# Kernel optimization log

Hardware: AMD Instinct MI355X
Metric: run time of the kernel (lower is better)

The kernel has to match this reference:

```python
import jax, jax.numpy as jnp
import numpy as np

B, N, D, HEAD = 16, 1024, 512, 256  # hidden_size=512, gcn_layer=2 -> head_dim=256


def _xavier(key, shape):
    lim = (6.0 / (shape[0] + shape[-1])) ** 0.5
    return jax.random.uniform(key, shape, jnp.float32, -lim, lim)


def setup_inputs() -> dict:
    key = jax.random.key(0)
    ks = jax.random.split(key, 10)
    fi_lim = (6.0 / (D + 1)) ** 0.5
    return {
        "x": jax.random.normal(ks[0], (B, N, D), jnp.float32),
        "tp_w": _xavier(ks[1], (D, D)), "tp_b": jnp.zeros((D,), jnp.float32),
        "tc_w": _xavier(ks[2], (D, D)), "tc_b": jnp.zeros((D,), jnp.float32),
        "fi_w": jax.random.uniform(ks[3], (D,), jnp.float32, -fi_lim, fi_lim),
        "bil_w": _xavier(ks[4], (D, D)),
        "gcn_w0": _xavier(ks[5], (D, HEAD)), "gcn_b0": jnp.zeros((HEAD,), jnp.float32),
        "gcn_w1": _xavier(ks[6], (D + HEAD, HEAD)), "gcn_b1": jnp.zeros((HEAD,), jnp.float32),
        "out_w": _xavier(ks[7], (D, D)), "out_b": jnp.zeros((D,), jnp.float32),
    }


def reference(x, tp_w, tp_b, tc_w, tc_b, fi_w, bil_w,
              gcn_w0, gcn_b0, gcn_w1, gcn_b1, out_w, out_b):
    Bb, Nn, Dd = x.shape
    # ---- StructInduction: matrix-tree latent structure ----
    tp = jnp.tanh(x @ tp_w + tp_b)                      # [B,N,D]
    tc = jnp.tanh(x @ tc_w + tc_b)                      # [B,N,D]
    # original expands BOTH tp and tc along dim 2 -> f_ij[b,i,j] = s[b,i]
    s = jnp.einsum('bnd,de,bne->bn', tp, bil_w, tc)     # [B,N]
    f_i = jnp.exp(x @ fi_w)                             # [B,N] root scores
    eye = jnp.eye(Nn, dtype=x.dtype)
    A = jnp.exp(s)[:, :, None] * (1.0 - eye)            # [B,N,N], zero diagonal
    col_sum = A.sum(axis=1)                             # [B,N] sum over dim 1
    L = -A + col_sum[:, None, :] * eye                  # Laplacian
    L = L.at[:, 0, :].set(f_i)                          # replace row 0 with root scores
    Linv = jnp.linalg.inv(L)                            # [B,N,N]
    d0 = f_i * Linv[:, :, 0]                            # [B,N]
    diag = jnp.diagonal(Linv, axis1=-2, axis2=-1)       # [B,N]
    tmp1 = A * diag[:, None, :]                         # A[b,i,j]*Linv_diag[b,j]
    tmp2 = A * jnp.swapaxes(Linv, 1, 2)                 # A[b,i,j]*Linv[b,j,i]
    mask1 = jnp.concatenate([jnp.zeros((Nn, 1), x.dtype),
                             jnp.ones((Nn, Nn - 1), x.dtype)], axis=1)  # zero col 0
    mask2 = mask1.T                                     # zero row 0
    dx = mask1 * tmp1 - mask2 * tmp2                    # [B,N,N]
    d = jnp.concatenate([d0[:, None, :], dx], axis=1)   # [B,N+1,N]
    df = jnp.swapaxes(d, 1, 2)                          # [B,N,N+1]
    adj = df[:, :, 1:]                                  # [B,N,N] latent adjacency
    # ---- GraphConvLayer (self_loop=True, dropout = identity / eval) ----
    denom = adj.sum(axis=2, keepdims=True) + 1.0        # [B,N,1]
    outputs = x
    cache = [x]
    outs = []
    for (W, b) in ((gcn_w0, gcn_b0), (gcn_w1, gcn_b1)):
        Ax = adj @ outputs                              # [B,N,in_dim]
        AxW = (Ax @ W + b) + (outputs @ W + b)          # neighbor + self loop
        g = jax.nn.relu(AxW / denom)                    # [B,N,HEAD]
        cache.append(g)
        outputs = jnp.concatenate(cache, axis=2)        # densely connected
        outs.append(g)
    gcn_out = jnp.concatenate(outs, axis=2) + x         # [B,N,D] residual
    return gcn_out @ out_w + out_b
```

## Files before the change

kernel.cpp:

```cpp
#include <hip/hip_runtime.h>
#include <cmath>

#define BN   16384
#define DD   512
#define HEADN 256

typedef unsigned short ushort;
typedef short short8 __attribute__((ext_vector_type(8)));
typedef float floatx4 __attribute__((ext_vector_type(4)));
typedef unsigned short ushort4v __attribute__((ext_vector_type(4)));
typedef unsigned short ushort8v __attribute__((ext_vector_type(8)));

__device__ __forceinline__ ushort f2bf(float v) {
    unsigned int u = __float_as_uint(v);
    unsigned int r = u + 0x7FFFu + ((u >> 16) & 1u);
    return (ushort)(r >> 16);
}
__device__ __forceinline__ float bf2f(ushort u) {
    return __uint_as_float(((unsigned int)u) << 16);
}
__device__ __forceinline__ float tanh_fast(float x) {
    float xc = fminf(fmaxf(x, -15.0f), 15.0f);
    float e = __expf(2.0f * xc);
    return (e - 1.0f) * __builtin_amdgcn_rcpf(e + 1.0f);
}

template <int TM, int TN, int BK, int KK, int EPI>
__global__ __launch_bounds__(256) void gemm_lds(
    const ushort* __restrict__ A, int lda,
    const ushort* __restrict__ Bt, int N,
    const float* __restrict__ bias,
    const float* __restrict__ denom,
    const ushort* __restrict__ tcb, int tcld,
    float* __restrict__ s_arr,
    void* __restrict__ Cout, int ldc,
    const ushort* __restrict__ xgb, int xoff, ushort* __restrict__ gout)
{
    constexpr int WGM = (TN == 64 && TM == 128) ? 4 : 2;
    constexpr int WGN = 4 / WGM;
    constexpr int MI = TM / (WGM * 16);
    constexpr int NI = TN / (WGN * 16);
    constexpr int KSTEPS = BK / 32;
    constexpr int ROWS = TM + TN;
    constexpr int CPR = BK / 8;
    constexpr int CPT = (ROWS * CPR) / 256;
    constexpr int MT = 16384 / TM;
    constexpr int MT_PER_BAND = MT / 8;
    constexpr int NK = KK / BK;
    __shared__ ushort S[2 * ROWS * BK];

    const int g = blockIdx.x;
    const int band = g & 7, within = g >> 3;
    const int nt = within / MT_PER_BAND;
    const int mt = band * MT_PER_BAND + (within - nt * MT_PER_BAND);
    const int m0 = mt * TM, n0 = nt * TN;
    const int w = threadIdx.x >> 6, L = threadIdx.x & 63;
    const int wr0 = ((WGN == 2) ? (w >> 1) : w) * (MI * 16);
    const int wc0 = ((WGN == 2) ? (w & 1) : 0) * (NI * 16);
    const int lrow = L & 15, quad = L >> 4;

    const ushort* gbase[CPT];
#pragma unroll
    for (int rr = 0; rr < CPT; ++rr) {
        const int chunk = rr * 256 + (w << 6) + L;
        const int row = chunk / CPR, slot = chunk % CPR;
        const int ca = slot ^ ((row >> 1) & (CPR - 1));
        gbase[rr] = (row < TM)
            ? A  + (size_t)(m0 + row) * lda    + (ca << 3)
            : Bt + (size_t)(n0 + row - TM) * KK + (ca << 3);
    }

    floatx4 zero4 = {0.0f, 0.0f, 0.0f, 0.0f};
    floatx4 acc[MI][NI];
#pragma unroll
    for (int i = 0; i < MI; ++i)
#pragma unroll
        for (int j = 0; j < NI; ++j) acc[i][j] = zero4;

    auto stage = [&](int buf, int k0) {
        ushort* Sd = S + buf * (ROWS * BK);
#pragma unroll
        for (int rr = 0; rr < CPT; ++rr) {
            __builtin_amdgcn_global_load_lds(
                (const __attribute__((address_space(1))) unsigned int*)(gbase[rr] + k0),
                (__attribute__((address_space(3))) unsigned int*)(Sd + (rr * 256 + (w << 6)) * 8),
                16, 0, 0);
        }
    };

    stage(0, 0);
#pragma unroll
    for (int kk = 0; kk < NK; ++kk) {
        __syncthreads();
        if (kk + 1 < NK) stage((kk + 1) & 1, (kk + 1) * BK);

        const ushort* Sc = S + (kk & 1) * (ROWS * BK);
        short8 af[KSTEPS][MI], bfr[KSTEPS][NI];
#pragma unroll
        for (int ks = 0; ks < KSTEPS; ++ks) {
#pragma unroll
            for (int mi = 0; mi < MI; ++mi) {
                const int row = wr0 + (mi << 4) + lrow;
                const int slot = ((ks << 2) + quad) ^ ((row >> 1) & (CPR - 1));
                af[ks][mi] = *(const short8*)(Sc + row * BK + (slot << 3));
            }
#pragma unroll
            for (int ni = 0; ni < NI; ++ni) {
                const int row = TM + wc0 + (ni << 4) + lrow;
                const int slot = ((ks << 2) + quad) ^ ((row >> 1) & (CPR - 1));
                bfr[ks][ni] = *(const short8*)(Sc + row * BK + (slot << 3));
            }
        }
#pragma unroll
        for (int ks = 0; ks < KSTEPS; ++ks)
#pragma unroll
            for (int mi = 0; mi < MI; ++mi)
#pragma unroll
                for (int ni = 0; ni < NI; ++ni)
                    acc[mi][ni] = __builtin_amdgcn_mfma_f32_16x16x32_bf16(
                        af[ks][mi], bfr[ks][ni], acc[mi][ni], 0, 0, 0);
    }

    if constexpr (EPI == 3) {
#pragma unroll
        for (int mi = 0; mi < MI; ++mi) {
            float rs[4] = {0.f, 0.f, 0.f, 0.f};
#pragma unroll
            for (int ni = 0; ni < NI; ++ni) {
                const int gc = n0 + wc0 + (ni << 4) + lrow;
#pragma unroll
                for (int p = 0; p < 4; ++p) {
                    const int gr = m0 + wr0 + (mi << 4) + (quad << 2) + p;
                    rs[p] += acc[mi][ni][p] * bf2f(tcb[(size_t)gr * tcld + gc]);
                }
            }
#pragma unroll
            for (int p = 0; p < 4; ++p)
#pragma unroll
                for (int o = 1; o < 16; o <<= 1) rs[p] += __shfl_xor(rs[p], o);
            if (lrow == 0) {
#pragma unroll
                for (int p = 0; p < 4; ++p)
                    atomicAdd(s_arr + m0 + wr0 + (mi << 4) + (quad << 2) + p, rs[p]);
            }
        }
    } else {
#pragma unroll
        for (int mi = 0; mi < MI; ++mi) {
#pragma unroll
            for (int p = 0; p < 4; ++p) {
                const int gr = m0 + wr0 + (mi << 4) + (quad << 2) + p;
                const float rdv = (EPI == 2) ? __builtin_amdgcn_rcpf(denom[gr]) : 1.0f;
#pragma unroll
                for (int ni = 0; ni < NI; ++ni) {
                    const int gc = n0 + wc0 + (ni << 4) + lrow;
                    const float v = acc[mi][ni][p];
                    if constexpr (EPI == 0) {
                        ((float*)Cout)[(size_t)gr * ldc + gc] = v + bias[gc];
                    } else if constexpr (EPI == 1) {
                        ((ushort*)Cout)[(size_t)gr * ldc + gc] = f2bf(tanh_fast(v + bias[gc]));
                    } else {
                        float u = (v + 2.0f * bias[gc]) * rdv;
                        u = u > 0.0f ? u : 0.0f;
                        if (Cout)
                            ((ushort*)Cout)[(size_t)gr * ldc + gc] = f2bf(u);
                        if (gout)
                            gout[(size_t)gr * 512 + xoff + gc] =
                                f2bf(u + bf2f(xgb[(size_t)gr * 512 + xoff + gc]));
                    }
                }
            }
        }
    }
}

__global__ __launch_bounds__(256) void prep_k(
    const float* __restrict__ x, const float* __restrict__ fiw,
    ushort* __restrict__ xb, float* __restrict__ fdot,
    const float* __restrict__ tp_w, const float* __restrict__ tc_w,
    const float* __restrict__ bilw, const float* __restrict__ ow,
    const float* __restrict__ w0, const float* __restrict__ w1,
    const float* __restrict__ tp_b, const float* __restrict__ tc_b,
    ushort* __restrict__ tptcwT, ushort* __restrict__ bilwT,
    ushort* __restrict__ owT, ushort* __restrict__ w0T,
    ushort* __restrict__ w1T, float* __restrict__ bias2)
{
    const int blk0 = blockIdx.x;
    if (blk0 < 4096) {
        const int wv = threadIdx.x >> 6, L = threadIdx.x & 63;
        const int r = (blk0 << 2) + wv;
        const float* xr = x + (size_t)r * DD;
        const int c0 = L << 3;
        float4 v0 = *(const float4*)(xr + c0);
        float4 v1 = *(const float4*)(xr + c0 + 4);
        float4 f0 = *(const float4*)(fiw + c0);
        float4 f1 = *(const float4*)(fiw + c0 + 4);
        float d = v0.x * f0.x + v0.y * f0.y + v0.z * f0.z + v0.w * f0.w
                + v1.x * f1.x + v1.y * f1.y + v1.z * f1.z + v1.w * f1.w;
        ushort8v o;
        o[0] = f2bf(v0.x); o[1] = f2bf(v0.y); o[2] = f2bf(v0.z); o[3] = f2bf(v0.w);
        o[4] = f2bf(v1.x); o[5] = f2bf(v1.y); o[6] = f2bf(v1.z); o[7] = f2bf(v1.w);
        *(ushort8v*)(xb + (size_t)r * DD + c0) = o;
#pragma unroll
        for (int off = 32; off > 0; off >>= 1) d += __shfl_xor(d, off);
        if (L == 0) fdot[r] = d;
        return;
    }
    const int blk = blk0 - 4096;
    if (blk >= 1344) {
        for (int i = threadIdx.x; i < 512; i += 256) {
            bias2[i] = tp_b[i];
            bias2[512 + i] = tc_b[i];
        }
        return;
    }
    const float* W; ushort* Wt; int K, N, local;
    if (blk < 256)       { W = tp_w; Wt = tptcwT;              K = 512; N = 512; local = blk; }
    else if (blk < 512)  { W = tc_w; Wt = tptcwT + 512 * 512;  K = 512; N = 512; local = blk - 256; }
    else if (blk < 768)  { W = bilw; Wt = bilwT;               K = 512; N = 512; local = blk - 512; }
    else if (blk < 1024) { W = ow;   Wt = owT;                 K = 512; N = 512; local = blk - 768; }
    else if (blk < 1152) { W = w0;   Wt = w0T;                 K = 512; N = 256; local = blk - 1024; }
    else                 { W = w1;   Wt = w1T;                 K = 768; N = 256; local = blk - 1152; }

    __shared__ float t[32][33];
    const int nb = N >> 5;
    const int kb = local / nb, nbb = local % nb;
    const int k0 = kb << 5, n0 = nbb << 5;
    const int c = threadIdx.x & 31, r = threadIdx.x >> 5;
#pragma unroll
    for (int i = 0; i < 4; ++i)
        t[r + 8 * i][c] = W[(size_t)(k0 + r + 8 * i) * N + n0 + c];
    __syncthreads();
#pragma unroll
    for (int i = 0; i < 4; ++i)
        Wt[(size_t)(n0 + r + 8 * i) * K + k0 + c] = f2bf(t[c][r + 8 * i]);
}

__global__ __launch_bounds__(1024) void finalize_k(
    const float* __restrict__ s_arr, const float* __restrict__ fdot,
    float* __restrict__ a, float* __restrict__ f,
    float* __restrict__ Sb, float* __restrict__ Hb, float* __restrict__ den)
{
    __shared__ float redS[16], redH[16];
    __shared__ float Hsh;
    const int b = blockIdx.x, t = threadIdx.x;
    const int r = (b << 10) + t;
    const float av = __expf(s_arr[r]), fv = __expf(fdot[r]);
    a[r] = av; f[r] = fv;
    float s1 = av, s2 = av * fv;
#pragma unroll
    for (int o = 32; o > 0; o >>= 1) { s1 += __shfl_xor(s1, o); s2 += __shfl_xor(s2, o); }
    if ((t & 63) == 0) { redS[t >> 6] = s1; redH[t >> 6] = s2; }
    __syncthreads();
    if (t == 0) {
        float S = 0.f, H = 0.f;
        for (int i = 0; i < 16; ++i) { S += redS[i]; H += redH[i]; }
        Sb[b] = S; Hb[b] = H; Hsh = H;
    }
    __syncthreads();
    den[r] = 2.0f - av * fv * __builtin_amdgcn_rcpf(Hsh);
}

__global__ __launch_bounds__(256) void batch_pq(
    const ushort* __restrict__ V, const float* __restrict__ a, const float* __restrict__ f,
    float* __restrict__ P, float* __restrict__ Q, int C)
{
    __shared__ float redP[256][4];
    __shared__ float redQ[256][4];
    const int b = blockIdx.x >> 4;
    const int chunk = blockIdx.x & 15;
    const int c4cnt = C >> 2;
    const int rg = 256 / c4cnt;
    const int c4 = threadIdx.x & (c4cnt - 1);
    const int sub = threadIdx.x / c4cnt;
    const ushort* Vb = V + (size_t)b * 1024 * C;
    const float* ab = a + (b << 10);
    const float* fb = f + (b << 10);
    const int n0 = chunk << 6;
    float4 p = {0, 0, 0, 0}, q = {0, 0, 0, 0};
    for (int n = n0 + sub; n < n0 + 64; n += rg) {
        const float av = ab[n], afv = av * fb[n];
        ushort4v u = *(const ushort4v*)(Vb + (size_t)n * C + (c4 << 2));
        float4 v = {bf2f(u[0]), bf2f(u[1]), bf2f(u[2]), bf2f(u[3])};
        p.x += av * v.x; p.y += av * v.y; p.z += av * v.z; p.w += av * v.w;
        q.x += afv * v.x; q.y += afv * v.y; q.z += afv * v.z; q.w += afv * v.w;
    }
    redP[threadIdx.x][0] = p.x; redP[threadIdx.x][1] = p.y;
    redP[threadIdx.x][2] = p.z; redP[threadIdx.x][3] = p.w;
    redQ[threadIdx.x][0] = q.x; redQ[threadIdx.x][1] = q.y;
    redQ[threadIdx.x][2] = q.z; redQ[threadIdx.x][3] = q.w;
    __syncthreads();
    if (sub == 0) {
        for (int s = 1; s < rg; ++s) {
            const int t2 = threadIdx.x + s * c4cnt;
            p.x += redP[t2][0]; p.y += redP[t2][1]; p.z += redP[t2][2]; p.w += redP[t2][3];
            q.x += redQ[t2][0]; q.y += redQ[t2][1]; q.z += redQ[t2][2]; q.w += redQ[t2][3];
        }
        float* Pp = P + b * C + (c4 << 2);
        float* Qp = Q + b * C + (c4 << 2);
        atomicAdd(Pp + 0, p.x); atomicAdd(Pp + 1, p.y);
        atomicAdd(Pp + 2, p.z); atomicAdd(Pp + 3, p.w);
        atomicAdd(Qp + 0, q.x); atomicAdd(Qp + 1, q.y);
        atomicAdd(Qp + 2, q.z); atomicAdd(Qp + 3, q.w);
    }
}

__global__ __launch_bounds__(256) void mix_k(
    const ushort* __restrict__ V, const float* __restrict__ P, const float* __restrict__ Q,
    const float* __restrict__ a, const float* __restrict__ f,
    const float* __restrict__ Sb, const float* __restrict__ Hb,
    ushort* __restrict__ outb, int C, int ldo, int co)
{
    const int idx = blockIdx.x * 256 + threadIdx.x;
    const int c4c = C >> 2;
    const int r = idx / c4c, c4 = idx - r * c4c;
    const int b = r >> 10;
    const float av = a[r], fv = f[r], S = Sb[b], H = Hb[b];
    const float rS = __builtin_amdgcn_rcpf(S);
    const float beta = av * rS * __builtin_amdgcn_rcpf(H);
    const float alpha = 1.0f - av * rS;
    const float cp = rS - beta * fv;
    ushort4v u = *(const ushort4v*)(V + (size_t)r * C + (c4 << 2));
    float4 v = {bf2f(u[0]), bf2f(u[1]), bf2f(u[2]), bf2f(u[3])};
    const float* Pp = P + b * C + (c4 << 2);
    const float* Qp = Q + b * C + (c4 << 2);
    ushort4v o;
    o[0] = f2bf(alpha * v.x + cp * Pp[0] + beta * Qp[0]);
    o[1] = f2bf(alpha * v.y + cp * Pp[1] + beta * Qp[1]);
    o[2] = f2bf(alpha * v.z + cp * Pp[2] + beta * Qp[2]);
    o[3] = f2bf(alpha * v.w + cp * Pp[3] + beta * Qp[3]);
    *(ushort4v*)(outb + (size_t)r * ldo + co + (c4 << 2)) = o;
}

extern "C" void kernel_launch(void* const* d_in, const int* in_sizes, int n_in,
                              void* d_out, int out_size, void* d_ws, size_t ws_size,
                              hipStream_t stream)
{
    (void)in_sizes; (void)n_in; (void)out_size; (void)ws_size;
    const float* x    = (const float*)d_in[0];
    const float* tp_w = (const float*)d_in[1];
    const float* tp_b = (const float*)d_in[2];
    const float* tc_w = (const float*)d_in[3];
    const float* tc_b = (const float*)d_in[4];
    const float* fi_w = (const float*)d_in[5];
    const float* bilw = (const float*)d_in[6];
    const float* w0   = (const float*)d_in[7];
    const float* b0   = (const float*)d_in[8];
    const float* w1   = (const float*)d_in[9];
    const float* b1   = (const float*)d_in[10];
    const float* ow   = (const float*)d_in[11];
    const float* ob   = (const float*)d_in[12];

    char* W = (char*)d_ws;
    ushort* xb    = (ushort*)W;
    ushort* gcnb  = xb;
    ushort* tptcb = (ushort*)(W + ((size_t)16 << 20));
    ushort* Hbuf  = tptcb;
    ushort* g0b   = (ushort*)(W + ((size_t)48 << 20));
    ushort* tptcwT= (ushort*)(W + ((size_t)56 << 20));
    ushort* bilwT = tptcwT + 524288;
    ushort* owT   = bilwT + 262144;
    ushort* w0T   = owT + 262144;
    ushort* w1T   = w0T + 131072;
    float*  bias2 = (float*)(w1T + 196608);
    float* stats  = (float*)(W + ((size_t)60 << 20));
    float* s_arr  = stats;
    float* P0     = s_arr + 16384;
    float* Q0     = P0 + 8192;
    float* P1     = Q0 + 8192;
    float* Q1     = P1 + 4096;
    float* fdot   = Q1 + 4096;
    float* arr_a  = fdot + BN;
    float* arr_f  = arr_a + BN;
    float* arr_den= arr_f + BN;
    float* Sb     = arr_den + BN;
    float* Hb     = Sb + 16;

    hipMemsetAsync(s_arr, 0, (16384 + 2 * 8192 + 2 * 4096) * sizeof(float), stream);

    prep_k<<<5441, 256, 0, stream>>>(x, fi_w, xb, fdot, tp_w, tc_w, bilw, ow, w0, w1,
                                     tp_b, tc_b, tptcwT, bilwT, owT, w0T, w1T, bias2);
    gemm_lds<128, 128, 32, 512, 1><<<1024, 256, 0, stream>>>(xb, 512, tptcwT, 1024, bias2,
        nullptr, nullptr, 0, nullptr, tptcb, 1024, nullptr, 0, nullptr);
    gemm_lds<128, 64, 32, 512, 3><<<1024, 256, 0, stream>>>(tptcb, 1024, bilwT, 512, nullptr,
        nullptr, tptcb + 512, 1024, s_arr, nullptr, 0, nullptr, 0, nullptr);
    finalize_k<<<16, 1024, 0, stream>>>(s_arr, fdot, arr_a, arr_f, Sb, Hb, arr_den);
    batch_pq<<<256, 256, 0, stream>>>(xb, arr_a, arr_f, P0, Q0, 512);
    mix_k<<<8192, 256, 0, stream>>>(xb, P0, Q0, arr_a, arr_f, Sb, Hb, Hbuf, 512, 768, 0);
    gemm_lds<64, 64, 64, 512, 2><<<1024, 256, 0, stream>>>(Hbuf, 768, w0T, 256, b0,
        arr_den, nullptr, 0, nullptr, g0b, 256, xb, 0, gcnb);
    batch_pq<<<256, 256, 0, stream>>>(g0b, arr_a, arr_f, P1, Q1, 256);
    mix_k<<<4096, 256, 0, stream>>>(g0b, P1, Q1, arr_a, arr_f, Sb, Hb, Hbuf, 256, 768, 512);
    gemm_lds<64, 64, 64, 768, 2><<<1024, 256, 0, stream>>>(Hbuf, 768, w1T, 256, b1,
        arr_den, nullptr, 0, nullptr, nullptr, 0, xb, 256, gcnb);
    gemm_lds<128, 64, 32, 512, 0><<<1024, 256, 0, stream>>>(gcnb, 512, owT, 512, ob,
        nullptr, nullptr, 0, nullptr, (float*)d_out, 512, nullptr, 0, nullptr);
}
```

Measured before the change: 242.4 us.

## Fuse finalize into batch_pq, fold memset into prep, retile bilinear and output GEMMs

Removes the finalize_k kernel. The exp of s and of fdot, plus the per-batch S/H sums, are now computed inside the first batch_pq, which accumulates the sums with atomics. The GCN epilogue recomputes the denominator from a, f and H instead of reading a stored array. The hipMemsetAsync is replaced by extra zeroing blocks in prep_k. The bilinear-score and output GEMMs move from 128x64 tiles to 64x64 tiles with twice as many blocks, and the warp layout is simplified to a fixed 2x2 grid. This cuts two launches and some memory traffic, but adds atomics and changes tile efficiency.

```diff
diff --git a/kernel.cpp b/kernel.cpp
--- a/kernel.cpp
+++ b/kernel.cpp
@@ -30,16 +30,15 @@
     const ushort* __restrict__ A, int lda,
     const ushort* __restrict__ Bt, int N,
     const float* __restrict__ bias,
-    const float* __restrict__ denom,
+    const float* __restrict__ af_arr, const float* __restrict__ f_arr,
+    const float* __restrict__ Hb_arr,
     const ushort* __restrict__ tcb, int tcld,
     float* __restrict__ s_arr,
     void* __restrict__ Cout, int ldc,
     const ushort* __restrict__ xgb, int xoff, ushort* __restrict__ gout)
 {
-    constexpr int WGM = (TN == 64 && TM == 128) ? 4 : 2;
-    constexpr int WGN = 4 / WGM;
-    constexpr int MI = TM / (WGM * 16);
-    constexpr int NI = TN / (WGN * 16);
+    constexpr int MI = TM / 32;
+    constexpr int NI = TN / 32;
     constexpr int KSTEPS = BK / 32;
     constexpr int ROWS = TM + TN;
     constexpr int CPR = BK / 8;
@@ -55,8 +54,8 @@
     const int mt = band * MT_PER_BAND + (within - nt * MT_PER_BAND);
     const int m0 = mt * TM, n0 = nt * TN;
     const int w = threadIdx.x >> 6, L = threadIdx.x & 63;
-    const int wr0 = ((WGN == 2) ? (w >> 1) : w) * (MI * 16);
-    const int wc0 = ((WGN == 2) ? (w & 1) : 0) * (NI * 16);
+    const int wr0 = (w >> 1) * (MI * 16);
+    const int wc0 = (w & 1) * (NI * 16);
     const int lrow = L & 15, quad = L >> 4;
 
     const ushort* gbase[CPT];
@@ -150,7 +149,12 @@
 #pragma unroll
             for (int p = 0; p < 4; ++p) {
                 const int gr = m0 + wr0 + (mi << 4) + (quad << 2) + p;
-                const float rdv = (EPI == 2) ? __builtin_amdgcn_rcpf(denom[gr]) : 1.0f;
+                float rdv = 1.0f;
+                if constexpr (EPI == 2) {
+                    const float dv = 2.0f - af_arr[gr] * f_arr[gr]
+                                     * __builtin_amdgcn_rcpf(Hb_arr[gr >> 10]);
+                    rdv = __builtin_amdgcn_rcpf(dv);
+                }
 #pragma unroll
                 for (int ni = 0; ni < NI; ++ni) {
                     const int gc = n0 + wc0 + (ni << 4) + lrow;
@@ -183,7 +187,8 @@
     const float* __restrict__ tp_b, const float* __restrict__ tc_b,
     ushort* __restrict__ tptcwT, ushort* __restrict__ bilwT,
     ushort* __restrict__ owT, ushort* __restrict__ w0T,
-    ushort* __restrict__ w1T, float* __restrict__ bias2)
+    ushort* __restrict__ w1T, float* __restrict__ bias2,
+    float* __restrict__ zstats, int zcount)
 {
     const int blk0 = blockIdx.x;
     if (blk0 < 4096) {
@@ -206,6 +211,11 @@
         if (L == 0) fdot[r] = d;
         return;
     }
+    if (blk0 >= 5441) {
+        for (int i = (blk0 - 5441) * 256 + threadIdx.x; i < zcount; i += 16 * 256)
+            zstats[i] = 0.0f;
+        return;
+    }
     const int blk = blk0 - 4096;
     if (blk >= 1344) {
         for (int i = threadIdx.x; i < 512; i += 256) {
@@ -236,33 +246,12 @@
         Wt[(size_t)(n0 + r + 8 * i) * K + k0 + c] = f2bf(t[c][r + 8 * i]);
 }
 
-__global__ __launch_bounds__(1024) void finalize_k(
+template <int COMPUTE_AF>
+__global__ __launch_bounds__(256) void batch_pq(
+    const ushort* __restrict__ V,
     const float* __restrict__ s_arr, const float* __restrict__ fdot,
     float* __restrict__ a, float* __restrict__ f,
-    float* __restrict__ Sb, float* __restrict__ Hb, float* __restrict__ den)
-{
-    __shared__ float redS[16], redH[16];
-    __shared__ float Hsh;
-    const int b = blockIdx.x, t = threadIdx.x;
-    const int r = (b << 10) + t;
-    const float av = __expf(s_arr[r]), fv = __expf(fdot[r]);
-    a[r] = av; f[r] = fv;
-    float s1 = av, s2 = av * fv;
-#pragma unroll
-    for (int o = 32; o > 0; o >>= 1) { s1 += __shfl_xor(s1, o); s2 += __shfl_xor(s2, o); }
-    if ((t & 63) == 0) { redS[t >> 6] = s1; redH[t >> 6] = s2; }
-    __syncthreads();
-    if (t == 0) {
-        float S = 0.f, H = 0.f;
-        for (int i = 0; i < 16; ++i) { S += redS[i]; H += redH[i]; }
-        Sb[b] = S; Hb[b] = H; Hsh = H;
-    }
-    __syncthreads();
-    den[r] = 2.0f - av * fv * __builtin_amdgcn_rcpf(Hsh);
-}
-
-__global__ __launch_bounds__(256) void batch_pq(
-    const ushort* __restrict__ V, const float* __restrict__ a, const float* __restrict__ f,
+    float* __restrict__ Sb, float* __restrict__ Hb,
     float* __restrict__ P, float* __restrict__ Q, int C)
 {
     __shared__ float redP[256][4];
@@ -274,16 +263,28 @@
     const int c4 = threadIdx.x & (c4cnt - 1);
     const int sub = threadIdx.x / c4cnt;
     const ushort* Vb = V + (size_t)b * 1024 * C;
-    const float* ab = a + (b << 10);
-    const float* fb = f + (b << 10);
     const int n0 = chunk << 6;
     float4 p = {0, 0, 0, 0}, q = {0, 0, 0, 0};
+    float sS = 0.0f, sH = 0.0f;
     for (int n = n0 + sub; n < n0 + 64; n += rg) {
-        const float av = ab[n], afv = av * fb[n];
+        const int gn = (b << 10) + n;
+        float av, fv;
+        if (COMPUTE_AF) {
+            av = __expf(s_arr[gn]); fv = __expf(fdot[gn]);
+            if (c4 == 0) { a[gn] = av; f[gn] = fv; }
+            sS += av; sH += av * fv;
+        } else {
+            av = a[gn]; fv = f[gn];
+        }
+        const float afv = av * fv;
         ushort4v u = *(const ushort4v*)(Vb + (size_t)n * C + (c4 << 2));
         float4 v = {bf2f(u[0]), bf2f(u[1]), bf2f(u[2]), bf2f(u[3])};
         p.x += av * v.x; p.y += av * v.y; p.z += av * v.z; p.w += av * v.w;
         q.x += afv * v.x; q.y += afv * v.y; q.z += afv * v.z; q.w += afv * v.w;
+    }
+    if (COMPUTE_AF && c4 == 0) {
+        atomicAdd(Sb + b, sS);
+        atomicAdd(Hb + b, sH);
     }
     redP[threadIdx.x][0] = p.x; redP[threadIdx.x][1] = p.y;
     redP[threadIdx.x][2] = p.z; redP[threadIdx.x][3] = p.w;
@@ -369,30 +370,28 @@
     float* Q0     = P0 + 8192;
     float* P1     = Q0 + 8192;
     float* Q1     = P1 + 4096;
-    float* fdot   = Q1 + 4096;
+    float* Sb     = Q1 + 4096;
+    float* Hb     = Sb + 16;
+    const int zcount = 16384 + 2 * 8192 + 2 * 4096 + 32;
+    float* fdot   = Hb + 16;
     float* arr_a  = fdot + BN;
     float* arr_f  = arr_a + BN;
-    float* arr_den= arr_f + BN;
-    float* Sb     = arr_den + BN;
-    float* Hb     = Sb + 16;
-
-    hipMemsetAsync(s_arr, 0, (16384 + 2 * 8192 + 2 * 4096) * sizeof(float), stream);
-
-    prep_k<<<5441, 256, 0, stream>>>(x, fi_w, xb, fdot, tp_w, tc_w, bilw, ow, w0, w1,
-                                     tp_b, tc_b, tptcwT, bilwT, owT, w0T, w1T, bias2);
+
+    prep_k<<<5457, 256, 0, stream>>>(x, fi_w, xb, fdot, tp_w, tc_w, bilw, ow, w0, w1,
+                                     tp_b, tc_b, tptcwT, bilwT, owT, w0T, w1T, bias2,
+                                     s_arr, zcount);
     gemm_lds<128, 128, 32, 512, 1><<<1024, 256, 0, stream>>>(xb, 512, tptcwT, 1024, bias2,
-        nullptr, nullptr, 0, nullptr, tptcb, 1024, nullptr, 0, nullptr);
-    gemm_lds<128, 64, 32, 512, 3><<<1024, 256, 0, stream>>>(tptcb, 1024, bilwT, 512, nullptr,
-        nullptr, tptcb + 512, 1024, s_arr, nullptr, 0, nullptr, 0, nullptr);
-    finalize_k<<<16, 1024, 0, stream>>>(s_arr, fdot, arr_a, arr_f, Sb, Hb, arr_den);
-    batch_pq<<<256, 256, 0, stream>>>(xb, arr_a, arr_f, P0, Q0, 512);
+        nullptr, nullptr, nullptr, nullptr, 0, nullptr, tptcb, 1024, nullptr, 0, nullptr);
+    gemm_lds<64, 64, 64, 512, 3><<<2048, 256, 0, stream>>>(tptcb, 1024, bilwT, 512, nullptr,
+        nullptr, nullptr, nullptr, tptcb + 512, 1024, s_arr, nullptr, 0, nullptr, 0, nullptr);
+    batch_pq<1><<<256, 256, 0, stream>>>(xb, s_arr, fdot, arr_a, arr_f, Sb, Hb, P0, Q0, 512);
     mix_k<<<8192, 256, 0, stream>>>(xb, P0, Q0, arr_a, arr_f, Sb, Hb, Hbuf, 512, 768, 0);
     gemm_lds<64, 64, 64, 512, 2><<<1024, 256, 0, stream>>>(Hbuf, 768, w0T, 256, b0,
-        arr_den, nullptr, 0, nullptr, g0b, 256, xb, 0, gcnb);
-    batch_pq<<<256, 256, 0, stream>>>(g0b, arr_a, arr_f, P1, Q1, 256);
+        arr_a, arr_f, Hb, nullptr, 0, nullptr, g0b, 256, xb, 0, gcnb);
+    batch_pq<0><<<256, 256, 0, stream>>>(g0b, nullptr, nullptr, arr_a, arr_f, nullptr, nullptr, P1, Q1, 256);
     mix_k<<<4096, 256, 0, stream>>>(g0b, P1, Q1, arr_a, arr_f, Sb, Hb, Hbuf, 256, 768, 512);
     gemm_lds<64, 64, 64, 768, 2><<<1024, 256, 0, stream>>>(Hbuf, 768, w1T, 256, b1,
-        arr_den, nullptr, 0, nullptr, nullptr, 0, xb, 256, gcnb);
-    gemm_lds<128, 64, 32, 512, 0><<<1024, 256, 0, stream>>>(gcnb, 512, owT, 512, ob,
-        nullptr, nullptr, 0, nullptr, (float*)d_out, 512, nullptr, 0, nullptr);
-}
+        arr_a, arr_f, Hb, nullptr, 0, nullptr, nullptr, 0, xb, 256, gcnb);
+    gemm_lds<64, 64, 64, 512, 0><<<2048, 256, 0, stream>>>(gcnb, 512, owT, 512, ob,
+        nullptr, nullptr, nullptr, nullptr, 0, nullptr, (float*)d_out, 512, nullptr, 0, nullptr);
+}
```

Measured after the change: 250.6 us. 3.4% more time.
